# Performance work log

Hardware: AMD Instinct MI355X
Metric: run time of the kernel (lower is better)

The kernel has to match this reference:

```python
import jax, jax.numpy as jnp
import numpy as np

B, L, A, F, E, P = 64, 50, 256, 8, 64, 4096
NF = A // 2  # friendly agents occupy slots [0, NF); unauth [NF, A)


def setup_inputs() -> dict:
    key = jax.random.key(0)
    ks = jax.random.split(key, 12)
    traj = jax.random.normal(ks[0], (B, L, A, F), dtype=jnp.float32)
    # roles: first half friendly (0), second half unauthorized (1)
    roles = jnp.concatenate([jnp.zeros((B, NF), jnp.int32), jnp.ones((B, A - NF), jnp.int32)], axis=1)
    pf = jax.random.randint(ks[1], (B, P), 0, NF, dtype=jnp.int32)          # friendly agent ids
    pu = jax.random.randint(ks[2], (B, P), NF, A, dtype=jnp.int32)          # unauth agent ids
    pairs = jnp.stack([pf, pu], axis=-1)                                    # [B, P, 2]
    s = 1.0 / np.sqrt(L * F)
    enc_f_W = jax.random.normal(ks[3], (L * F, E), jnp.float32) * s
    enc_f_b = jnp.zeros((E,), jnp.float32)
    enc_u_W = jax.random.normal(ks[4], (L * F, E), jnp.float32) * s
    enc_u_b = jnp.zeros((E,), jnp.float32)
    cls_W1 = jax.random.normal(ks[5], (4 * E, E), jnp.float32) / np.sqrt(4 * E)
    cls_b1 = jnp.zeros((E,), jnp.float32)
    cls_W2 = jax.random.normal(ks[6], (E, 1), jnp.float32) / np.sqrt(E)
    cls_b2 = jnp.zeros((1,), jnp.float32)
    return {"batch_trajectories": traj, "batch_roles": roles, "pairs": pairs,
            "enc_f_W": enc_f_W, "enc_f_b": enc_f_b, "enc_u_W": enc_u_W, "enc_u_b": enc_u_b,
            "cls_W1": cls_W1, "cls_b1": cls_b1, "cls_W2": cls_W2, "cls_b2": cls_b2}


def reference(batch_trajectories, batch_roles, pairs,
              enc_f_W, enc_f_b, enc_u_W, enc_u_b,
              cls_W1, cls_b1, cls_W2, cls_b2) -> jnp.ndarray:
    # per-agent flattened trajectories: [B, A, L*F]
    x = batch_trajectories.transpose(0, 2, 1, 3).reshape(B, A, L * F)
    # roles are fixed by construction: [0, NF) friendly, [NF, A) unauthorized
    emb_f_all = x[:, :NF] @ enc_f_W + enc_f_b   # [B, NF, E]
    emb_u_all = x[:, NF:] @ enc_u_W + enc_u_b   # [B, A-NF, E]
    f_idx = pairs[..., 0]                       # [B, P] in [0, NF)
    u_idx = pairs[..., 1] - NF                  # [B, P] in [0, A-NF)
    ef = jnp.take_along_axis(emb_f_all, f_idx[..., None], axis=1)  # [B, P, E]
    eu = jnp.take_along_axis(emb_u_all, u_idx[..., None], axis=1)  # [B, P, E]
    rel = jnp.concatenate([ef, eu, jnp.abs(ef - eu), ef * eu], axis=-1)  # [B, P, 4E]
    h = jax.nn.relu(rel @ cls_W1 + cls_b1)
    logits = h @ cls_W2 + cls_b2               # [B, P, 1]
    return logits
```

## Files before the change

kernel.cpp:

```cpp
#include <hip/hip_runtime.h>
#include <hip/hip_bf16.h>

#define B_  64
#define L_  50
#define A_  256
#define F_  8
#define E_  64
#define P_  4096
#define NF_ 128

typedef __attribute__((ext_vector_type(8))) short bhalf8;
typedef __attribute__((ext_vector_type(4))) float f32x4;

union BF { bhalf8 v; unsigned u[4]; short s[8]; };

static __device__ __forceinline__ unsigned pk2(float lo, float hi) {
    __hip_bfloat162 h = __float22bfloat162_rn(float2{lo, hi});
    union { __hip_bfloat162 h; unsigned u; } c; c.h = h;
    return c.u;
}


#define ENC_KSTEPS 13
#define FRAG_TOTAL 136
#define W1_FRAG_OFF (104 * 64)
#define EMB_OFF 65536

__global__ __launch_bounds__(256) void wprep_kernel(
    const float* __restrict__ Wf, const float* __restrict__ Wu,
    const float* __restrict__ W1, uint4* __restrict__ frags) {
    const int gid = blockIdx.x * 256 + threadIdx.x;
    if (gid >= FRAG_TOTAL * 64) return;
    const int fid = gid >> 6, lane = gid & 63;
    const int r = lane & 15, g = lane >> 4;
    const float* W; int s, t, K;
    if (fid < 104) {
        const int role = fid / 52, sf = fid % 52;
        s = sf >> 2; t = sf & 3; W = role ? Wu : Wf; K = 400;
    } else {
        const int st = fid - 104;
        s = st >> 2; t = st & 3; W = W1; K = 256;
    }
    float v[8];
#pragma unroll
    for (int j = 0; j < 8; ++j) {
        const int k = 32 * s + 8 * g + j;
        v[j] = (k < K) ? W[k * E_ + 16 * t + r] : 0.f;
    }
    uint4 u;
    u.x = pk2(v[0], v[1]); u.y = pk2(v[2], v[3]);
    u.z = pk2(v[4], v[5]); u.w = pk2(v[6], v[7]);
    frags[gid] = u;
}

__global__ __launch_bounds__(256, 2) void enc_kernel(
    const float* __restrict__ traj, const uint4* __restrict__ frags,
    const float* __restrict__ bf_, const float* __restrict__ bu_,
    float* __restrict__ emb) {
    const int tid = threadIdx.x;
    const int lane = tid & 63;
    const int r = lane & 15, g = lane >> 4;
    const int mt = blockIdx.x * 4 + (tid >> 6);
    const int b = mt >> 4;
    const int a0 = (mt & 15) * 16;
    const int role = (a0 >= NF_) ? 1 : 0;
    const uint4* __restrict__ wfr = frags + role * 52 * 64;

    float4 xa[ENC_KSTEPS], xb[ENC_KSTEPS];
#pragma unroll
    for (int s = 0; s < ENC_KSTEPS; ++s) {
        if (s < 12 || g < 2) {
            const float* p = traj + (((size_t)b * L_ + 4 * s + g) * A_ + a0 + r) * F_;
            xa[s] = *(const float4*)p;
            xb[s] = *(const float4*)(p + 4);
        } else {
            xa[s] = float4{0.f, 0.f, 0.f, 0.f};
            xb[s] = float4{0.f, 0.f, 0.f, 0.f};
        }
    }

    f32x4 acc[4];
#pragma unroll
    for (int t = 0; t < 4; ++t) acc[t] = (f32x4){0.f, 0.f, 0.f, 0.f};

#pragma unroll
    for (int s = 0; s < ENC_KSTEPS; ++s) {
        BF a;
        a.u[0] = pk2(xa[s].x, xa[s].y); a.u[1] = pk2(xa[s].z, xa[s].w);
        a.u[2] = pk2(xb[s].x, xb[s].y); a.u[3] = pk2(xb[s].z, xb[s].w);
#pragma unroll
        for (int t = 0; t < 4; ++t) {
            BF w; *(uint4*)w.u = wfr[(s * 4 + t) * 64 + lane];
            acc[t] = __builtin_amdgcn_mfma_f32_16x16x32_bf16(a.v, w.v, acc[t], 0, 0, 0);
        }
    }

    const float* __restrict__ bias = role ? bu_ : bf_;
    float bv[4];
#pragma unroll
    for (int t = 0; t < 4; ++t) bv[t] = bias[16 * t + r];
#pragma unroll
    for (int t = 0; t < 4; ++t)
#pragma unroll
        for (int reg = 0; reg < 4; ++reg) {
            const int row = a0 + 4 * g + reg;
            emb[((size_t)b * A_ + row) * E_ + 16 * t + r] = acc[t][reg] + bv[t];
        }
}

#define CLS_BLOCKS 4096
__global__ __launch_bounds__(256, 2) void cls_kernel(
    const float* __restrict__ emb, const int* __restrict__ pairs,
    const uint4* __restrict__ frags, const float* __restrict__ b1,
    const float* __restrict__ W2, const float* __restrict__ b2,
    float* __restrict__ out) {
    const int tid = threadIdx.x;
    const int lane = tid & 63;
    const int r = lane & 15;
    const int g = lane >> 4;

    __shared__ uint4 wlds[2048];
#pragma unroll
    for (int it = 0; it < 8; ++it)
        wlds[tid + it * 256] = frags[W1_FRAG_OFF + tid + it * 256];
    __syncthreads();

    float b1v[4], w2v[4];
#pragma unroll
    for (int t = 0; t < 4; ++t) { b1v[t] = b1[16 * t + r]; w2v[t] = W2[16 * t + r]; }
    const float bias2 = b2[0];

    const int tile = blockIdx.x * 4 + (tid >> 6);
    const int m0 = tile * 16;
    const int b = m0 >> 12;
    const int p = (m0 & (P_ - 1)) + r;
    const int2 pr = ((const int2*)pairs)[(size_t)b * P_ + p];
    const float* ef = emb + ((size_t)b * A_ + pr.x) * E_ + 8 * g;
    const float* eu = emb + ((size_t)b * A_ + pr.y) * E_ + 8 * g;

    const float4 f0a = *(const float4*)(ef);
    const float4 f0b = *(const float4*)(ef + 4);
    const float4 f1a = *(const float4*)(ef + 32);
    const float4 f1b = *(const float4*)(ef + 36);
    const float4 u0a = *(const float4*)(eu);
    const float4 u0b = *(const float4*)(eu + 4);
    const float4 u1a = *(const float4*)(eu + 32);
    const float4 u1b = *(const float4*)(eu + 36);

    auto pack = [](float4 x, float4 y) {
        BF o;
        o.u[0] = pk2(x.x, x.y); o.u[1] = pk2(x.z, x.w);
        o.u[2] = pk2(y.x, y.y); o.u[3] = pk2(y.z, y.w);
        return o;
    };
    auto adiff = [](float4 a, float4 b) {
        float4 o; o.x = fabsf(a.x - b.x); o.y = fabsf(a.y - b.y);
        o.z = fabsf(a.z - b.z); o.w = fabsf(a.w - b.w); return o;
    };
    auto mul4 = [](float4 a, float4 b) {
        float4 o; o.x = a.x * b.x; o.y = a.y * b.y;
        o.z = a.z * b.z; o.w = a.w * b.w; return o;
    };
    BF aF[8];
    aF[0] = pack(f0a, f0b);
    aF[1] = pack(f1a, f1b);
    aF[2] = pack(u0a, u0b);
    aF[3] = pack(u1a, u1b);
    aF[4] = pack(adiff(f0a, u0a), adiff(f0b, u0b));
    aF[5] = pack(adiff(f1a, u1a), adiff(f1b, u1b));
    aF[6] = pack(mul4(f0a, u0a), mul4(f0b, u0b));
    aF[7] = pack(mul4(f1a, u1a), mul4(f1b, u1b));

    f32x4 acc[4];
#pragma unroll
    for (int t = 0; t < 4; ++t) acc[t] = (f32x4){0.f, 0.f, 0.f, 0.f};
#pragma unroll
    for (int s = 0; s < 8; ++s) {
#pragma unroll
        for (int t = 0; t < 4; ++t) {
            BF bw; *(uint4*)bw.u = wlds[(s * 4 + t) * 64 + lane];
            acc[t] = __builtin_amdgcn_mfma_f32_16x16x32_bf16(aF[s].v, bw.v, acc[t], 0, 0, 0);
        }
    }

    float s0 = 0.f, s1 = 0.f, s2 = 0.f, s3 = 0.f;
#pragma unroll
    for (int t = 0; t < 4; ++t) {
        float h;
        h = acc[t][0] + b1v[t]; h = h > 0.f ? h : 0.f; s0 += h * w2v[t];
        h = acc[t][1] + b1v[t]; h = h > 0.f ? h : 0.f; s1 += h * w2v[t];
        h = acc[t][2] + b1v[t]; h = h > 0.f ? h : 0.f; s2 += h * w2v[t];
        h = acc[t][3] + b1v[t]; h = h > 0.f ? h : 0.f; s3 += h * w2v[t];
    }
#pragma unroll
    for (int m = 1; m < 16; m <<= 1) {
        s0 += __shfl_xor(s0, m);
        s1 += __shfl_xor(s1, m);
        s2 += __shfl_xor(s2, m);
        s3 += __shfl_xor(s3, m);
    }
    if (r < 4) {
        const float v = (r == 0) ? s0 : (r == 1) ? s1 : (r == 2) ? s2 : s3;
        out[m0 + 4 * g + r] = v + bias2;
    }
}

extern "C" void kernel_launch(void* const* d_in, const int* in_sizes, int n_in,
                              void* d_out, int out_size, void* d_ws, size_t ws_size,
                              hipStream_t stream) {
    const float* traj = (const float*)d_in[0];
    const int*   pairs = (const int*)d_in[2];
    const float* Wf = (const float*)d_in[3];
    const float* bf = (const float*)d_in[4];
    const float* Wu = (const float*)d_in[5];
    const float* bu = (const float*)d_in[6];
    const float* W1 = (const float*)d_in[7];
    const float* b1 = (const float*)d_in[8];
    const float* W2 = (const float*)d_in[9];
    const float* b2 = (const float*)d_in[10];
    float* out = (float*)d_out;
    uint4* frags = (uint4*)d_ws;
    float* emb = (float*)d_ws + EMB_OFF;

    wprep_kernel<<<dim3((FRAG_TOTAL * 64 + 255) / 256), dim3(256), 0, stream>>>(Wf, Wu, W1, frags);
    enc_kernel<<<dim3(256), dim3(256), 0, stream>>>(traj, frags, bf, bu, emb);
    cls_kernel<<<dim3(CLS_BLOCKS), dim3(256), 0, stream>>>(emb, pairs, frags, b1, W2, b2, out);
}
```

Before: 126.9 us.

## Split encoder K dimension across two waves with reduction kernel; batch classifier tiles per wave

The encoder GEMM's 400-long reduction is split into two halves of 25 timesteps each. Twice as many waves each compute a partial product, and a new reduction kernel sums the two partials and adds the bias. This doubles encoder parallelism (512 blocks instead of 256) and shortens each wave's serial dependency chain, at the cost of an extra kernel launch and extra partial-buffer traffic. The classifier now handles four tiles per wave with a quarter of the blocks, which amortizes the per-block LDS weight load.

After: 123.2 us. 2.9% less time.

```diff
diff --git a/kernel.cpp b/kernel.cpp
--- a/kernel.cpp
+++ b/kernel.cpp
@@ -8,6 +8,7 @@
 #define E_  64
 #define P_  4096
 #define NF_ 128
+#define NEMB (B_ * A_ * E_)
 
 typedef __attribute__((ext_vector_type(8))) short bhalf8;
 typedef __attribute__((ext_vector_type(4))) float f32x4;
@@ -21,10 +22,10 @@
 }
 
 
-#define ENC_KSTEPS 13
-#define FRAG_TOTAL 136
-#define W1_FRAG_OFF (104 * 64)
-#define EMB_OFF 65536
+#define ENC_KSTEPS 7
+#define FRAG_TOTAL 144
+#define W1_FRAG_OFF (112 * 64)
+#define PART_OFF 65536
 
 __global__ __launch_bounds__(256) void wprep_kernel(
     const float* __restrict__ Wf, const float* __restrict__ Wu,
@@ -33,19 +34,26 @@
     if (gid >= FRAG_TOTAL * 64) return;
     const int fid = gid >> 6, lane = gid & 63;
     const int r = lane & 15, g = lane >> 4;
-    const float* W; int s, t, K;
-    if (fid < 104) {
-        const int role = fid / 52, sf = fid % 52;
-        s = sf >> 2; t = sf & 3; W = role ? Wu : Wf; K = 400;
+    float v[8];
+    if (fid < 112) {
+        const int role = fid / 56;
+        const int rem = fid % 56;
+        const int half = rem / 28;
+        const int s = (rem % 28) >> 2, t = rem & 3;
+        const float* W = role ? Wu : Wf;
+#pragma unroll
+        for (int j = 0; j < 8; ++j) {
+            const int kl = 32 * s + 8 * g + j;
+            v[j] = (kl < 200) ? W[(200 * half + kl) * E_ + 16 * t + r] : 0.f;
+        }
     } else {
-        const int st = fid - 104;
-        s = st >> 2; t = st & 3; W = W1; K = 256;
-    }
-    float v[8];
-#pragma unroll
-    for (int j = 0; j < 8; ++j) {
-        const int k = 32 * s + 8 * g + j;
-        v[j] = (k < K) ? W[k * E_ + 16 * t + r] : 0.f;
+        const int st = fid - 112;
+        const int s = st >> 2, t = st & 3;
+#pragma unroll
+        for (int j = 0; j < 8; ++j) {
+            const int k = 32 * s + 8 * g + j;
+            v[j] = W1[k * E_ + 16 * t + r];
+        }
     }
     uint4 u;
     u.x = pk2(v[0], v[1]); u.y = pk2(v[2], v[3]);
@@ -55,22 +63,24 @@
 
 __global__ __launch_bounds__(256, 2) void enc_kernel(
     const float* __restrict__ traj, const uint4* __restrict__ frags,
-    const float* __restrict__ bf_, const float* __restrict__ bu_,
-    float* __restrict__ emb) {
+    float* __restrict__ part) {
     const int tid = threadIdx.x;
     const int lane = tid & 63;
     const int r = lane & 15, g = lane >> 4;
-    const int mt = blockIdx.x * 4 + (tid >> 6);
+    const int wid = blockIdx.x * 4 + (tid >> 6);
+    const int mt = wid >> 1;
+    const int half = wid & 1;
     const int b = mt >> 4;
     const int a0 = (mt & 15) * 16;
     const int role = (a0 >= NF_) ? 1 : 0;
-    const uint4* __restrict__ wfr = frags + role * 52 * 64;
+    const uint4* __restrict__ wfr = frags + (role * 56 + half * 28) * 64;
 
     float4 xa[ENC_KSTEPS], xb[ENC_KSTEPS];
 #pragma unroll
     for (int s = 0; s < ENC_KSTEPS; ++s) {
-        if (s < 12 || g < 2) {
-            const float* p = traj + (((size_t)b * L_ + 4 * s + g) * A_ + a0 + r) * F_;
+        if (4 * s + g < 25) {
+            const int l = 25 * half + 4 * s + g;
+            const float* p = traj + (((size_t)b * L_ + l) * A_ + a0 + r) * F_;
             xa[s] = *(const float4*)p;
             xb[s] = *(const float4*)(p + 4);
         } else {
@@ -95,20 +105,32 @@
         }
     }
 
-    const float* __restrict__ bias = role ? bu_ : bf_;
-    float bv[4];
-#pragma unroll
-    for (int t = 0; t < 4; ++t) bv[t] = bias[16 * t + r];
 #pragma unroll
     for (int t = 0; t < 4; ++t)
 #pragma unroll
         for (int reg = 0; reg < 4; ++reg) {
             const int row = a0 + 4 * g + reg;
-            emb[((size_t)b * A_ + row) * E_ + 16 * t + r] = acc[t][reg] + bv[t];
-        }
-}
-
-#define CLS_BLOCKS 4096
+            part[(size_t)half * NEMB + ((size_t)b * A_ + row) * E_ + 16 * t + r] = acc[t][reg];
+        }
+}
+
+__global__ __launch_bounds__(256) void red_kernel(
+    const float* __restrict__ part, const float* __restrict__ bf_,
+    const float* __restrict__ bu_, float* __restrict__ emb) {
+    const int idx = (blockIdx.x * 256 + threadIdx.x) * 4;
+    const float4 p0 = *(const float4*)(part + idx);
+    const float4 p1 = *(const float4*)(part + NEMB + idx);
+    const int a = (idx >> 6) & (A_ - 1);
+    const float* bias = (a < NF_) ? bf_ : bu_;
+    const float4 bv = *(const float4*)(bias + (idx & 63));
+    float4 o;
+    o.x = p0.x + p1.x + bv.x; o.y = p0.y + p1.y + bv.y;
+    o.z = p0.z + p1.z + bv.z; o.w = p0.w + p1.w + bv.w;
+    *(float4*)(emb + idx) = o;
+}
+
+#define CLS_BLOCKS 1024
+#define TPW 4
 __global__ __launch_bounds__(256, 2) void cls_kernel(
     const float* __restrict__ emb, const int* __restrict__ pairs,
     const uint4* __restrict__ frags, const float* __restrict__ b1,
@@ -129,79 +151,82 @@
 #pragma unroll
     for (int t = 0; t < 4; ++t) { b1v[t] = b1[16 * t + r]; w2v[t] = W2[16 * t + r]; }
     const float bias2 = b2[0];
-
-    const int tile = blockIdx.x * 4 + (tid >> 6);
-    const int m0 = tile * 16;
-    const int b = m0 >> 12;
-    const int p = (m0 & (P_ - 1)) + r;
-    const int2 pr = ((const int2*)pairs)[(size_t)b * P_ + p];
-    const float* ef = emb + ((size_t)b * A_ + pr.x) * E_ + 8 * g;
-    const float* eu = emb + ((size_t)b * A_ + pr.y) * E_ + 8 * g;
-
-    const float4 f0a = *(const float4*)(ef);
-    const float4 f0b = *(const float4*)(ef + 4);
-    const float4 f1a = *(const float4*)(ef + 32);
-    const float4 f1b = *(const float4*)(ef + 36);
-    const float4 u0a = *(const float4*)(eu);
-    const float4 u0b = *(const float4*)(eu + 4);
-    const float4 u1a = *(const float4*)(eu + 32);
-    const float4 u1b = *(const float4*)(eu + 36);
-
-    auto pack = [](float4 x, float4 y) {
-        BF o;
-        o.u[0] = pk2(x.x, x.y); o.u[1] = pk2(x.z, x.w);
-        o.u[2] = pk2(y.x, y.y); o.u[3] = pk2(y.z, y.w);
-        return o;
-    };
-    auto adiff = [](float4 a, float4 b) {
-        float4 o; o.x = fabsf(a.x - b.x); o.y = fabsf(a.y - b.y);
-        o.z = fabsf(a.z - b.z); o.w = fabsf(a.w - b.w); return o;
-    };
-    auto mul4 = [](float4 a, float4 b) {
-        float4 o; o.x = a.x * b.x; o.y = a.y * b.y;
-        o.z = a.z * b.z; o.w = a.w * b.w; return o;
-    };
-    BF aF[8];
-    aF[0] = pack(f0a, f0b);
-    aF[1] = pack(f1a, f1b);
-    aF[2] = pack(u0a, u0b);
-    aF[3] = pack(u1a, u1b);
-    aF[4] = pack(adiff(f0a, u0a), adiff(f0b, u0b));
-    aF[5] = pack(adiff(f1a, u1a), adiff(f1b, u1b));
-    aF[6] = pack(mul4(f0a, u0a), mul4(f0b, u0b));
-    aF[7] = pack(mul4(f1a, u1a), mul4(f1b, u1b));
-
-    f32x4 acc[4];
-#pragma unroll
-    for (int t = 0; t < 4; ++t) acc[t] = (f32x4){0.f, 0.f, 0.f, 0.f};
-#pragma unroll
-    for (int s = 0; s < 8; ++s) {
+    const int wid = blockIdx.x * 4 + (tid >> 6);
+
+    for (int ti = 0; ti < TPW; ++ti) {
+        const int tile = wid * TPW + ti;
+        const int m0 = tile * 16;
+        const int b = m0 >> 12;
+        const int p = (m0 & (P_ - 1)) + r;
+        const int2 pr = ((const int2*)pairs)[(size_t)b * P_ + p];
+        const float* ef = emb + ((size_t)b * A_ + pr.x) * E_ + 8 * g;
+        const float* eu = emb + ((size_t)b * A_ + pr.y) * E_ + 8 * g;
+
+        const float4 f0a = *(const float4*)(ef);
+        const float4 f0b = *(const float4*)(ef + 4);
+        const float4 f1a = *(const float4*)(ef + 32);
+        const float4 f1b = *(const float4*)(ef + 36);
+        const float4 u0a = *(const float4*)(eu);
+        const float4 u0b = *(const float4*)(eu + 4);
+        const float4 u1a = *(const float4*)(eu + 32);
+        const float4 u1b = *(const float4*)(eu + 36);
+
+        auto pack = [](float4 x, float4 y) {
+            BF o;
+            o.u[0] = pk2(x.x, x.y); o.u[1] = pk2(x.z, x.w);
+            o.u[2] = pk2(y.x, y.y); o.u[3] = pk2(y.z, y.w);
+            return o;
+        };
+        auto adiff = [](float4 a, float4 b) {
+            float4 o; o.x = fabsf(a.x - b.x); o.y = fabsf(a.y - b.y);
+            o.z = fabsf(a.z - b.z); o.w = fabsf(a.w - b.w); return o;
+        };
+        auto mul4 = [](float4 a, float4 b) {
+            float4 o; o.x = a.x * b.x; o.y = a.y * b.y;
+            o.z = a.z * b.z; o.w = a.w * b.w; return o;
+        };
+        BF aF[8];
+        aF[0] = pack(f0a, f0b);
+        aF[1] = pack(f1a, f1b);
+        aF[2] = pack(u0a, u0b);
+        aF[3] = pack(u1a, u1b);
+        aF[4] = pack(adiff(f0a, u0a), adiff(f0b, u0b));
+        aF[5] = pack(adiff(f1a, u1a), adiff(f1b, u1b));
+        aF[6] = pack(mul4(f0a, u0a), mul4(f0b, u0b));
+        aF[7] = pack(mul4(f1a, u1a), mul4(f1b, u1b));
+
+        f32x4 acc[4];
+#pragma unroll
+        for (int t = 0; t < 4; ++t) acc[t] = (f32x4){0.f, 0.f, 0.f, 0.f};
+#pragma unroll
+        for (int s = 0; s < 8; ++s) {
+#pragma unroll
+            for (int t = 0; t < 4; ++t) {
+                BF bw; *(uint4*)bw.u = wlds[(s * 4 + t) * 64 + lane];
+                acc[t] = __builtin_amdgcn_mfma_f32_16x16x32_bf16(aF[s].v, bw.v, acc[t], 0, 0, 0);
+            }
+        }
+
+        float s0 = 0.f, s1 = 0.f, s2 = 0.f, s3 = 0.f;
 #pragma unroll
         for (int t = 0; t < 4; ++t) {
-            BF bw; *(uint4*)bw.u = wlds[(s * 4 + t) * 64 + lane];
-            acc[t] = __builtin_amdgcn_mfma_f32_16x16x32_bf16(aF[s].v, bw.v, acc[t], 0, 0, 0);
-        }
-    }
-
-    float s0 = 0.f, s1 = 0.f, s2 = 0.f, s3 = 0.f;
-#pragma unroll
-    for (int t = 0; t < 4; ++t) {
-        float h;
-        h = acc[t][0] + b1v[t]; h = h > 0.f ? h : 0.f; s0 += h * w2v[t];
-        h = acc[t][1] + b1v[t]; h = h > 0.f ? h : 0.f; s1 += h * w2v[t];
-        h = acc[t][2] + b1v[t]; h = h > 0.f ? h : 0.f; s2 += h * w2v[t];
-        h = acc[t][3] + b1v[t]; h = h > 0.f ? h : 0.f; s3 += h * w2v[t];
-    }
-#pragma unroll
-    for (int m = 1; m < 16; m <<= 1) {
-        s0 += __shfl_xor(s0, m);
-        s1 += __shfl_xor(s1, m);
-        s2 += __shfl_xor(s2, m);
-        s3 += __shfl_xor(s3, m);
-    }
-    if (r < 4) {
-        const float v = (r == 0) ? s0 : (r == 1) ? s1 : (r == 2) ? s2 : s3;
-        out[m0 + 4 * g + r] = v + bias2;
+            float h;
+            h = acc[t][0] + b1v[t]; h = h > 0.f ? h : 0.f; s0 += h * w2v[t];
+            h = acc[t][1] + b1v[t]; h = h > 0.f ? h : 0.f; s1 += h * w2v[t];
+            h = acc[t][2] + b1v[t]; h = h > 0.f ? h : 0.f; s2 += h * w2v[t];
+            h = acc[t][3] + b1v[t]; h = h > 0.f ? h : 0.f; s3 += h * w2v[t];
+        }
+#pragma unroll
+        for (int m = 1; m < 16; m <<= 1) {
+            s0 += __shfl_xor(s0, m);
+            s1 += __shfl_xor(s1, m);
+            s2 += __shfl_xor(s2, m);
+            s3 += __shfl_xor(s3, m);
+        }
+        if (r < 4) {
+            const float v = (r == 0) ? s0 : (r == 1) ? s1 : (r == 2) ? s2 : s3;
+            out[m0 + 4 * g + r] = v + bias2;
+        }
     }
 }
 
@@ -220,9 +245,11 @@
     const float* b2 = (const float*)d_in[10];
     float* out = (float*)d_out;
     uint4* frags = (uint4*)d_ws;
-    float* emb = (float*)d_ws + EMB_OFF;
+    float* part = (float*)d_ws + PART_OFF;
+    float* emb  = (float*)d_ws + PART_OFF + 2 * NEMB;
 
     wprep_kernel<<<dim3((FRAG_TOTAL * 64 + 255) / 256), dim3(256), 0, stream>>>(Wf, Wu, W1, frags);
-    enc_kernel<<<dim3(256), dim3(256), 0, stream>>>(traj, frags, bf, bu, emb);
+    enc_kernel<<<dim3(512), dim3(256), 0, stream>>>(traj, frags, part);
+    red_kernel<<<dim3(1024), dim3(256), 0, stream>>>(part, bf, bu, emb);
     cls_kernel<<<dim3(CLS_BLOCKS), dim3(256), 0, stream>>>(emb, pairs, frags, b1, W2, b2, out);
 }
```
